# Kernel tuning notes

Hardware: AMD Instinct MI355X
Metric: run time of the kernel (lower is better)

The kernel has to match this reference:

```python
import jax, jax.numpy as jnp
import numpy as np

DIM = 1024
HEADS = 16
HEAD_DIM = DIM // HEADS
THRESH = 0.29514
SHARP = 15.0
LN_EPS = 1e-5
NORM_EPS = 1e-12


def setup_inputs() -> dict:
    key = jax.random.key(0)
    ks = jax.random.split(key, 8)
    s = 1.0 / np.sqrt(DIM)
    sg = 1.0 / np.sqrt(HEAD_DIM)
    return {
        "x": jax.random.normal(ks[0], (2, 2048, DIM), dtype=jnp.float32),
        "Wq": jax.random.uniform(ks[1], (DIM, DIM), jnp.float32, -s, s),
        "Wk": jax.random.uniform(ks[2], (DIM, DIM), jnp.float32, -s, s),
        "Wv": jax.random.uniform(ks[3], (DIM, DIM), jnp.float32, -s, s),
        "gq": jax.random.uniform(ks[4], (HEAD_DIM,), jnp.float32, -sg, sg),
        "gk": jax.random.uniform(ks[5], (HEAD_DIM,), jnp.float32, -sg, sg),
        "Wo": jax.random.uniform(ks[6], (DIM, DIM), jnp.float32, -s, s),
        "bo": jax.random.uniform(ks[7], (DIM,), jnp.float32, -s, s),
        "ln_w": jnp.ones((DIM,), jnp.float32),
        "ln_b": jnp.zeros((DIM,), jnp.float32),
    }


def _l2norm(t):
    # F.normalize: t / max(||t||_2, eps)
    n = jnp.sqrt(jnp.sum(t * t, axis=-1, keepdims=True))
    return t / jnp.maximum(n, NORM_EPS)


def reference(x, Wq, Wk, Wv, gq, gk, Wo, bo, ln_w, ln_b):
    B, T, D = x.shape
    # LayerNorm over last dim
    mu = jnp.mean(x, axis=-1, keepdims=True)
    var = jnp.mean((x - mu) ** 2, axis=-1, keepdims=True)
    x_norm = (x - mu) / jnp.sqrt(var + LN_EPS) * ln_w + ln_b

    def split_heads(t):  # [B,T,D] -> [B,H,T,hd]
        return t.reshape(B, T, HEADS, HEAD_DIM).transpose(0, 2, 1, 3)

    q = _l2norm(split_heads(x_norm @ Wq))
    k = _l2norm(split_heads(x_norm @ Wk))
    v = split_heads(x @ Wv)  # note: v uses un-normalized x, as in source

    align = jnp.einsum("bhtd,bhsd->bhts", q, k)  # cosine alignment
    resonance = jax.nn.sigmoid((align - THRESH) * SHARP)
    gate_q = jnp.einsum("bhtd,d->bht", q, gq)
    gate_k = jnp.einsum("bhsd,d->bhs", k, gk)
    modulation = resonance * gate_q[..., :, None] * gate_k[..., None, :]
    collapse = jnp.einsum("bhts,bhsd->bhtd", modulation, v)
    collapse = collapse.transpose(0, 2, 1, 3).reshape(B, T, D)
    return collapse @ Wo + bo
```

## Files before the change

### kernel.cpp

```cpp
#include <hip/hip_runtime.h>
#include <math.h>

#define DIM 1024
#define T_SEQ 2048
#define NBATCH 2
#define HEADS 16
#define HD 64
#define NTOK 4096
#define THRESH 0.29514f
#define SHARP 15.0f
#define LOG2E 1.4426950408889634f

typedef __attribute__((ext_vector_type(8))) short bf16x8;
typedef __attribute__((ext_vector_type(4))) float f32x4;
typedef __attribute__((ext_vector_type(4))) unsigned int u32x4;

__device__ __forceinline__ unsigned short f2b(float f) {
    unsigned int u = __float_as_uint(f);
    unsigned int r = (u + 0x7FFFu + ((u >> 16) & 1u)) >> 16;
    return (unsigned short)r;
}
__device__ __forceinline__ float b2f(unsigned short u) {
    return __uint_as_float(((unsigned int)u) << 16);
}
__device__ __forceinline__ unsigned int pack2_bf16(float lo, float hi) {
    unsigned int a = __float_as_uint(lo) + 0x8000u;
    unsigned int b = __float_as_uint(hi) + 0x8000u;
    return __builtin_amdgcn_perm(b, a, 0x07060302u);
}

__device__ __forceinline__ void async_cp16(const unsigned short* g, unsigned short* l) {
    __builtin_amdgcn_global_load_lds(
        (const __attribute__((address_space(1))) unsigned int*)g,
        (__attribute__((address_space(3))) unsigned int*)l, 16, 0, 0);
}

__global__ __launch_bounds__(256) void prep_kernel(
    const float* __restrict__ x, const float* __restrict__ lnw, const float* __restrict__ lnb,
    unsigned short* __restrict__ xnb, unsigned short* __restrict__ xb,
    const float* __restrict__ W0, const float* __restrict__ W1,
    const float* __restrict__ W2, const float* __restrict__ W3,
    unsigned short* __restrict__ T0, unsigned short* __restrict__ T1,
    unsigned short* __restrict__ T2, unsigned short* __restrict__ T3) {
    __shared__ float tile[64][65];
    if (blockIdx.x < 1024) {
        int row = blockIdx.x * 4 + (threadIdx.x >> 6);
        int lane = threadIdx.x & 63;
        const float4* xr = (const float4*)(x + (size_t)row * DIM);
        float4 v[4];
        float s = 0.f, ss = 0.f;
#pragma unroll
        for (int i = 0; i < 4; i++) {
            v[i] = xr[lane + i * 64];
            s += v[i].x + v[i].y + v[i].z + v[i].w;
            ss += v[i].x * v[i].x + v[i].y * v[i].y + v[i].z * v[i].z + v[i].w * v[i].w;
        }
#pragma unroll
        for (int off = 32; off; off >>= 1) {
            s += __shfl_xor(s, off);
            ss += __shfl_xor(ss, off);
        }
        float m = s * (1.f / DIM);
        float rstd = rsqrtf(ss * (1.f / DIM) - m * m + 1e-5f);
#pragma unroll
        for (int i = 0; i < 4; i++) {
            int e = (lane + i * 64) * 4;
            float4 lw = *(const float4*)&lnw[e];
            float4 lb = *(const float4*)&lnb[e];
            ushort4 un, ur;
            un.x = f2b((v[i].x - m) * rstd * lw.x + lb.x);
            un.y = f2b((v[i].y - m) * rstd * lw.y + lb.y);
            un.z = f2b((v[i].z - m) * rstd * lw.z + lb.z);
            un.w = f2b((v[i].w - m) * rstd * lw.w + lb.w);
            ur.x = f2b(v[i].x); ur.y = f2b(v[i].y); ur.z = f2b(v[i].z); ur.w = f2b(v[i].w);
            *(ushort4*)&xnb[(size_t)row * DIM + e] = un;
            *(ushort4*)&xb[(size_t)row * DIM + e] = ur;
        }
    } else {
        const int i = blockIdx.x - 1024;
        const int z = i >> 8;
        const int k0 = ((i >> 4) & 15) * 64, n0 = (i & 15) * 64;
        const float* W = (z == 0) ? W0 : (z == 1) ? W1 : (z == 2) ? W2 : W3;
        unsigned short* T = (z == 0) ? T0 : (z == 1) ? T1 : (z == 2) ? T2 : T3;
        const int r = threadIdx.x >> 3;
        const int c = (threadIdx.x & 7) * 8;
#pragma unroll
        for (int half = 0; half < 2; half++) {
            int rr = r + half * 32;
            float4 a = *(const float4*)&W[(size_t)(k0 + rr) * DIM + n0 + c];
            float4 b = *(const float4*)&W[(size_t)(k0 + rr) * DIM + n0 + c + 4];
            tile[rr][c + 0] = a.x; tile[rr][c + 1] = a.y; tile[rr][c + 2] = a.z; tile[rr][c + 3] = a.w;
            tile[rr][c + 4] = b.x; tile[rr][c + 5] = b.y; tile[rr][c + 6] = b.z; tile[rr][c + 7] = b.w;
        }
        __syncthreads();
#pragma unroll
        for (int half = 0; half < 2; half++) {
            int dd = r + half * 32;
            bf16x8 o;
#pragma unroll
            for (int j = 0; j < 8; j++) o[j] = (short)f2b(tile[c + j][dd]);
            *(bf16x8*)&T[(size_t)(n0 + dd) * DIM + k0 + c] = o;
        }
    }
}

template <int MODE>
__global__ __launch_bounds__(256) void gemm_mfma_kernel(
    const unsigned short* __restrict__ A0, const unsigned short* __restrict__ A2,
    const unsigned short* __restrict__ Bt0, const unsigned short* __restrict__ Bt1,
    const unsigned short* __restrict__ Bt2, const float* __restrict__ bias,
    const float* __restrict__ gq, const float* __restrict__ gk,
    unsigned short* __restrict__ Oq, unsigned short* __restrict__ Ok,
    unsigned short* __restrict__ Ov, float* __restrict__ gq_t, float* __restrict__ gk_t,
    float* __restrict__ Oout) {
    constexpr int NT = (MODE == 0) ? 4 : 2;
    constexpr int NBUF = (MODE == 0) ? 3 : 2;
    __shared__ __align__(16) unsigned short As[NBUF][128 * 32];
    __shared__ __align__(16) unsigned short Bs[NBUF][NT * 32 * 32];
    const int tid = threadIdx.x;
    const int lane = tid & 63, w = tid >> 6;
    const int l16 = lane & 15, quad = lane >> 4;
    const int wm = w >> 1, wn = w & 1;
    int m0, n0, z = 0;
    if constexpr (MODE == 0) {
        const int f = blockIdx.x + (blockIdx.y << 5) + (blockIdx.z << 8);
        const int ww = (f & 7) * 96 + (f >> 3);
        z = ww >> 8;
        m0 = ((ww >> 3) & 31) * 128;
        n0 = (ww & 7) * 128;
    } else {
        const int f = blockIdx.x + (blockIdx.y << 5);
        const int ww = (f & 7) * 64 + (f >> 3);
        m0 = (ww >> 4) * 128;
        n0 = (ww & 15) * 64;
    }
    const unsigned short* A;
    const unsigned short* Bt;
    if constexpr (MODE == 0) {
        A = (z == 2) ? A2 : A0;
        Bt = (z == 0) ? Bt0 : (z == 1) ? Bt1 : Bt2;
    } else {
        A = A0;
        Bt = Bt0;
    }
    f32x4 acc[4][NT] = {};
    const int kswz = (l16 >> 1) & 3;

    const int lin0 = tid, lin1 = 256 + tid;
    const int sm0 = lin0 >> 2, sk0 = (lin0 & 3) ^ ((sm0 >> 1) & 3);
    const int sm1 = lin1 >> 2, sk1 = (lin1 & 3) ^ ((sm1 >> 1) & 3);

    auto stage_async = [&](int kb, int k0) {
        async_cp16(Bt + (size_t)(n0 + sm0) * DIM + k0 + sk0 * 8, &Bs[kb][lin0 * 8]);
        if constexpr (MODE == 0) {
            async_cp16(Bt + (size_t)(n0 + sm1) * DIM + k0 + sk1 * 8, &Bs[kb][lin1 * 8]);
            async_cp16(A + (size_t)(m0 + sm0) * DIM + k0 + sk0 * 8, &As[kb][lin0 * 8]);
            async_cp16(A + (size_t)(m0 + sm1) * DIM + k0 + sk1 * 8, &As[kb][lin1 * 8]);
        }
    };

    bf16x8 pa0, pa1, pc0, pc1;
    auto loadA = [&](int k0) {
        const size_t o0 = (size_t)(m0 + sm0) * DIM + k0 + sk0 * 8;
        const size_t o1 = (size_t)(m0 + sm1) * DIM + k0 + sk1 * 8;
        pa0 = *(const bf16x8*)(A + o0);
        pc0 = *(const bf16x8*)(A2 + o0);
        pa1 = *(const bf16x8*)(A + o1);
        pc1 = *(const bf16x8*)(A2 + o1);
    };
    auto writeA = [&](int kb) {
        bf16x8 o0, o1;
#pragma unroll
        for (int j = 0; j < 8; j++) {
            o0[j] = (short)f2b(b2f((unsigned short)pa0[j]) + b2f((unsigned short)pc0[j]));
            o1[j] = (short)f2b(b2f((unsigned short)pa1[j]) + b2f((unsigned short)pc1[j]));
        }
        *(bf16x8*)(&As[kb][lin0 * 8]) = o0;
        *(bf16x8*)(&As[kb][lin1 * 8]) = o1;
    };

    auto compute = [&](int cur) {
        bf16x8 af[4], bfr[NT];
#pragma unroll
        for (int t = 0; t < 4; t++) {
            int ma = wm * 64 + t * 16 + l16;
            af[t] = *(const bf16x8*)(&As[cur][ma * 32 + ((quad ^ kswz) * 8)]);
        }
#pragma unroll
        for (int t = 0; t < NT; t++) {
            int nb = wn * (NT * 16) + t * 16 + l16;
            bfr[t] = *(const bf16x8*)(&Bs[cur][nb * 32 + ((quad ^ kswz) * 8)]);
        }
#pragma unroll
        for (int mt = 0; mt < 4; mt++)
#pragma unroll
            for (int nt = 0; nt < NT; nt++)
                acc[mt][nt] =
                    __builtin_amdgcn_mfma_f32_16x16x32_bf16(af[mt], bfr[nt], acc[mt][nt], 0, 0, 0);
    };

    if constexpr (MODE == 0) {
        stage_async(0, 0);
        stage_async(1, 32);
        int cur = 0, stg = 2;
        for (int ks = 0; ks < DIM / 32; ks++) {
            __builtin_amdgcn_s_barrier();
            if (ks + 2 < DIM / 32) {
                stage_async(stg, (ks + 2) * 32);
                asm volatile("s_waitcnt vmcnt(8)" ::: "memory");
            } else if (ks + 1 < DIM / 32) {
                asm volatile("s_waitcnt vmcnt(4)" ::: "memory");
            } else {
                asm volatile("s_waitcnt vmcnt(0)" ::: "memory");
            }
            __builtin_amdgcn_s_barrier();
            compute(cur);
            cur = (cur == 2) ? 0 : cur + 1;
            stg = (stg == 2) ? 0 : stg + 1;
        }
    } else {
        stage_async(0, 0);
        loadA(0);
        writeA(0);
        __syncthreads();
        for (int ks = 0; ks < DIM / 32; ks++) {
            const int cur = ks & 1;
            if (ks + 1 < DIM / 32) {
                stage_async(cur ^ 1, (ks + 1) * 32);
                loadA((ks + 1) * 32);
            }
            compute(cur);
            if (ks + 1 < DIM / 32) writeA(cur ^ 1);
            __syncthreads();
        }
    }

    if constexpr (MODE == 0) {
        const int h = (n0 + wn * 64) >> 6;
        if (z <= 1) {
            constexpr float QSCALE = -SHARP * LOG2E;
            const float* gvec = (z == 0) ? gq : gk;
            float* gate = (z == 0) ? gq_t : gk_t;
            unsigned short* O = (z == 0) ? Oq : Ok;
            const float oscale = (z == 0) ? QSCALE : 1.0f;
            float gv[4];
#pragma unroll
            for (int nt = 0; nt < 4; nt++) gv[nt] = gvec[nt * 16 + l16];
#pragma unroll
            for (int mt = 0; mt < 4; mt++) {
#pragma unroll
                for (int r = 0; r < 4; r++) {
                    float ss = 0.f;
#pragma unroll
                    for (int nt = 0; nt < 4; nt++) ss += acc[mt][nt][r] * acc[mt][nt][r];
#pragma unroll
                    for (int msk = 1; msk < 16; msk <<= 1) ss += __shfl_xor(ss, msk);
                    float rn = __builtin_amdgcn_rcpf(fmaxf(sqrtf(ss), 1e-12f));
                    float vn[4], gg = 0.f;
#pragma unroll
                    for (int nt = 0; nt < 4; nt++) {
                        vn[nt] = acc[mt][nt][r] * rn;
                        gg += vn[nt] * gv[nt];
                    }
#pragma unroll
                    for (int msk = 1; msk < 16; msk <<= 1) gg += __shfl_xor(gg, msk);
                    int tok = m0 + wm * 64 + mt * 16 + quad * 4 + r;
                    int b = tok >> 11, t = tok & 2047;
                    size_t rowbase = ((size_t)(b * HEADS + h) * T_SEQ + t) * HD;
#pragma unroll
                    for (int nt = 0; nt < 4; nt++)
                        O[rowbase + nt * 16 + l16] = f2b(vn[nt] * oscale);
                    if (l16 == 0) gate[(b * HEADS + h) * T_SEQ + t] = gg;
                }
            }
        } else {
#pragma unroll
            for (int mt = 0; mt < 4; mt++) {
#pragma unroll
                for (int r = 0; r < 4; r++) {
                    int tok = m0 + wm * 64 + mt * 16 + quad * 4 + r;
                    int b = tok >> 11, t = tok & 2047;
                    size_t rowbase = ((size_t)(b * HEADS + h) * T_SEQ + t) * HD;
#pragma unroll
                    for (int nt = 0; nt < 4; nt++)
                        Ov[rowbase + nt * 16 + l16] = f2b(acc[mt][nt][r]);
                }
            }
        }
    } else {
        float bias_r[NT];
#pragma unroll
        for (int nt = 0; nt < NT; nt++) bias_r[nt] = bias[n0 + wn * (NT * 16) + nt * 16 + l16];
#pragma unroll
        for (int mt = 0; mt < 4; mt++) {
#pragma unroll
            for (int r = 0; r < 4; r++) {
                int tok = m0 + wm * 64 + mt * 16 + quad * 4 + r;
#pragma unroll
                for (int nt = 0; nt < NT; nt++) {
                    int n = n0 + wn * (NT * 16) + nt * 16 + l16;
                    Oout[(size_t)tok * DIM + n] = acc[mt][nt][r] + bias_r[nt];
                }
            }
        }
    }
}

__global__ __launch_bounds__(256) void vtrans_kernel(const unsigned short* __restrict__ Vn,
                                                     const float* __restrict__ gk_t,
                                                     unsigned short* __restrict__ Vt) {
    __shared__ float tile[64][65];
    const int bh = blockIdx.y;
    const int t0 = blockIdx.x * 64;
    const int r = threadIdx.x >> 3;
    const int c = (threadIdx.x & 7) * 8;
    const unsigned short* src = Vn + (size_t)bh * T_SEQ * HD;
#pragma unroll
    for (int half = 0; half < 2; half++) {
        int rr = r + half * 32;
        float gkv = gk_t[bh * T_SEQ + t0 + rr];
        bf16x8 v = *(const bf16x8*)(src + (size_t)(t0 + rr) * HD + c);
#pragma unroll
        for (int j = 0; j < 8; j++) tile[rr][c + j] = b2f((unsigned short)v[j]) * gkv;
    }
    __syncthreads();
    unsigned short* dst = Vt + (size_t)bh * HD * T_SEQ;
#pragma unroll
    for (int half = 0; half < 2; half++) {
        int dd = r + half * 32;
        bf16x8 o;
#pragma unroll
        for (int j = 0; j < 8; j++) o[j] = (short)f2b(tile[c + j][dd]);
        *(bf16x8*)(dst + (size_t)dd * T_SEQ + t0 + c) = o;
    }
}

__global__ __launch_bounds__(256, 4) void attn_mfma_kernel(
    const unsigned short* __restrict__ Qn, const unsigned short* __restrict__ Kn,
    const unsigned short* __restrict__ Vt, const float* __restrict__ gateq,
    unsigned short* __restrict__ collp0, unsigned short* __restrict__ collp1) {
    __shared__ __align__(16) unsigned short Ks[2][64 * 64];
    __shared__ __align__(16) unsigned short VtL[2][64 * 64];
    const int tid = threadIdx.x;
    const int lane = tid & 63, w = tid >> 6;
    const int quad = lane >> 4, l16 = lane & 15;
    const int f = blockIdx.x + 16 * blockIdx.y + 256 * blockIdx.z;
    const int q_ = f >> 3;
    const int panel = (f & 7) * 8 + (q_ >> 4);
    const int t0 = (q_ & 15) * 128;
    const int h = panel & 15;
    const int zz = panel >> 4;
    const int b = zz >> 1, shalf = zz & 1;
    const int sbase = shalf * (T_SEQ / 2);
    const int bh = b * HEADS + h;
    const size_t base = (size_t)bh * T_SEQ * HD;
    constexpr float K0 = THRESH * SHARP * LOG2E;
    const f32x4 k0v = {K0, K0, K0, K0};

    int det0 = quad, det1 = quad + 4;
    asm("v_permlane16_swap_b32 %0, %1" : "+v"(det0), "+v"(det1));
    const bool flagA = (__builtin_amdgcn_readfirstlane(det0) == 0);

    bf16x8 fq[2][2];
#pragma unroll
    for (int mt = 0; mt < 2; mt++) {
        const unsigned short* qrow = Qn + base + (size_t)(t0 + w * 32 + mt * 16 + l16) * HD;
        fq[mt][0] = *(const bf16x8*)(qrow + quad * 8);
        fq[mt][1] = *(const bf16x8*)(qrow + 32 + quad * 8);
    }

    f32x4 oacc[4][2] = {};
    const int srow = tid >> 3;
    const int sgp = tid & 7;
    const int swz = l16 & 7;

    auto stage_chunk = [&](unsigned short* ksn, unsigned short* vtn, int s0) {
#pragma unroll
        for (int half = 0; half < 2; half++) {
            int row = srow + half * 32;
            int g = sgp ^ (row & 7);
            async_cp16(Kn + base + (size_t)(s0 + row) * HD + g * 8, ksn + row * 64 + sgp * 8);
            async_cp16(Vt + base + (size_t)row * T_SEQ + s0 + g * 8, vtn + row * 64 + sgp * 8);
        }
    };

    auto do_chunk = [&](const unsigned short* ksb, const unsigned short* vtb) {
#pragma unroll
        for (int kh = 0; kh < 2; kh++) {
            unsigned int p[2][2][2];
#pragma unroll
            for (int ct2 = 0; ct2 < 2; ct2++) {
                const int ct = 2 * kh + ct2;
                const unsigned short* krow = ksb + (ct * 16 + l16) * 64;
                bf16x8 fk0 = *(const bf16x8*)(krow + (quad ^ swz) * 8);
                bf16x8 fk1 = *(const bf16x8*)(krow + ((quad + 4) ^ swz) * 8);
#pragma unroll
                for (int mt = 0; mt < 2; mt++) {
                    __builtin_amdgcn_s_setprio(1);
                    f32x4 s1 =
                        __builtin_amdgcn_mfma_f32_16x16x32_bf16(fk0, fq[mt][0], k0v, 0, 0, 0);
                    f32x4 sacc =
                        __builtin_amdgcn_mfma_f32_16x16x32_bf16(fk1, fq[mt][1], s1, 0, 0, 0);
                    __builtin_amdgcn_s_setprio(0);
                    float w0 = __builtin_amdgcn_rcpf(1.f + __builtin_amdgcn_exp2f(sacc[0]));
                    float w1 = __builtin_amdgcn_rcpf(1.f + __builtin_amdgcn_exp2f(sacc[1]));
                    float w2 = __builtin_amdgcn_rcpf(1.f + __builtin_amdgcn_exp2f(sacc[2]));
                    float w3 = __builtin_amdgcn_rcpf(1.f + __builtin_amdgcn_exp2f(sacc[3]));
                    p[mt][ct2][0] = pack2_bf16(w0, w1);
                    p[mt][ct2][1] = pack2_bf16(w2, w3);
                }
            }
            int gv = (4 * kh + 2 * (quad & 1) + (quad >> 1)) ^ swz;
            bf16x8 fv[4];
#pragma unroll
            for (int dt = 0; dt < 4; dt++)
                fv[dt] = *(const bf16x8*)(vtb + (dt * 16 + l16) * 64 + gv * 8);
#pragma unroll
            for (int mt = 0; mt < 2; mt++) {
                unsigned int aL = p[mt][0][0], aH = p[mt][0][1];
                unsigned int bL = p[mt][1][0], bH = p[mt][1][1];
                asm("v_permlane16_swap_b32 %0, %1" : "+v"(aL), "+v"(bL));
                asm("v_permlane16_swap_b32 %0, %1" : "+v"(aH), "+v"(bH));
                u32x4 bt;
                if (flagA) {
                    bt.x = aL; bt.y = aH; bt.z = bL; bt.w = bH;
                } else {
                    bt.x = bL; bt.y = bH; bt.z = aL; bt.w = aH;
                }
                bf16x8 fs = __builtin_bit_cast(bf16x8, bt);
                __builtin_amdgcn_s_setprio(1);
#pragma unroll
                for (int dt = 0; dt < 4; dt++)
                    oacc[dt][mt] =
                        __builtin_amdgcn_mfma_f32_16x16x32_bf16(fv[dt], fs, oacc[dt][mt], 0, 0, 0);
                __builtin_amdgcn_s_setprio(0);
            }
        }
        __syncthreads();
    };

    stage_chunk(&Ks[0][0], &VtL[0][0], sbase);
    __syncthreads();

    for (int j = 0; j < T_SEQ / 256; j++) {
        stage_chunk(&Ks[1][0], &VtL[1][0], sbase + j * 128 + 64);
        do_chunk(&Ks[0][0], &VtL[0][0]);
        if (j + 1 < T_SEQ / 256) stage_chunk(&Ks[0][0], &VtL[0][0], sbase + j * 128 + 128);
        do_chunk(&Ks[1][0], &VtL[1][0]);
    }

    unsigned short* collp = shalf ? collp1 : collp0;
#pragma unroll
    for (int mt = 0; mt < 2; mt++) {
        int t = t0 + w * 32 + mt * 16 + l16;
        float gq_v = gateq[bh * T_SEQ + t];
        unsigned short* dst = collp + ((size_t)b * T_SEQ + t) * DIM + h * HD;
#pragma unroll
        for (int dt = 0; dt < 4; dt++) {
            ushort4 o;
            o.x = f2b(oacc[dt][mt][0] * gq_v);
            o.y = f2b(oacc[dt][mt][1] * gq_v);
            o.z = f2b(oacc[dt][mt][2] * gq_v);
            o.w = f2b(oacc[dt][mt][3] * gq_v);
            *(ushort4*)(dst + dt * 16 + quad * 4) = o;
        }
    }
}

extern "C" void kernel_launch(void* const* d_in, const int* in_sizes, int n_in,
                              void* d_out, int out_size, void* d_ws, size_t ws_size,
                              hipStream_t stream) {
    const float* x = (const float*)d_in[0];
    const float* Wq = (const float*)d_in[1];
    const float* Wk = (const float*)d_in[2];
    const float* Wv = (const float*)d_in[3];
    const float* gq = (const float*)d_in[4];
    const float* gk = (const float*)d_in[5];
    const float* Wo = (const float*)d_in[6];
    const float* bo = (const float*)d_in[7];
    const float* lnw = (const float*)d_in[8];
    const float* lnb = (const float*)d_in[9];
    float* out = (float*)d_out;

    unsigned short* ws = (unsigned short*)d_ws;
    unsigned short* xnb = ws;
    unsigned short* xb = xnb + (size_t)NTOK * DIM;
    unsigned short* Wqt = xb + (size_t)NTOK * DIM;
    unsigned short* Wkt = Wqt + (size_t)DIM * DIM;
    unsigned short* Wvt = Wkt + (size_t)DIM * DIM;
    unsigned short* Wot = Wvt + (size_t)DIM * DIM;
    unsigned short* Q16 = Wot + (size_t)DIM * DIM;
    unsigned short* K16 = Q16 + (size_t)NTOK * DIM;
    unsigned short* Vn = K16 + (size_t)NTOK * DIM;
    float* gq_t = (float*)(Vn + (size_t)NTOK * DIM);
    float* gk_t = gq_t + NBATCH * HEADS * T_SEQ;
    unsigned short* collb1 = (unsigned short*)(gk_t + NBATCH * HEADS * T_SEQ);
    unsigned short* Vt = xnb;
    unsigned short* collb0 = xb;

    prep_kernel<<<2048, 256, 0, stream>>>(x, lnw, lnb, xnb, xb, Wq, Wk, Wv, Wo, Wqt, Wkt, Wvt,
                                          Wot);
    gemm_mfma_kernel<0><<<dim3(NTOK / 128, DIM / 128, 3), 256, 0, stream>>>(
        xnb, xb, Wqt, Wkt, Wvt, nullptr, gq, gk, Q16, K16, Vn, gq_t, gk_t, nullptr);
    vtrans_kernel<<<dim3(T_SEQ / 64, NBATCH * HEADS), 256, 0, stream>>>(Vn, gk_t, Vt);
    attn_mfma_kernel<<<dim3(T_SEQ / 128, HEADS, NBATCH * 2), 256, 0, stream>>>(
        Q16, K16, Vt, gq_t, collb0, collb1);
    gemm_mfma_kernel<1><<<dim3(NTOK / 128, DIM / 64, 1), 256, 0, stream>>>(
        collb0, collb1, Wot, nullptr, nullptr, bo, nullptr, nullptr, nullptr, nullptr, nullptr,
        nullptr, nullptr, out);
}
```

Measured before the change: 222.1 us.

## Remove split-KV attention and partial-sum reduction in output projection GEMM

Attention blocks now iterate over the full key sequence instead of half, halving the grid and writing a single collapse buffer. The output-projection GEMM loads A via async copies directly rather than loading two partial buffers and adding them in registers. This removes the extra partial-buffer write/read and the add-on-load, at the cost of fewer attention blocks and lower parallelism/occupancy.

```diff
diff --git a/kernel.cpp b/kernel.cpp
--- a/kernel.cpp
+++ b/kernel.cpp
@@ -106,13 +106,13 @@
 
 template <int MODE>
 __global__ __launch_bounds__(256) void gemm_mfma_kernel(
-    const unsigned short* __restrict__ A0, const unsigned short* __restrict__ A2,
+    const unsigned short* __restrict__ A0,
     const unsigned short* __restrict__ Bt0, const unsigned short* __restrict__ Bt1,
     const unsigned short* __restrict__ Bt2, const float* __restrict__ bias,
     const float* __restrict__ gq, const float* __restrict__ gk,
     unsigned short* __restrict__ Oq, unsigned short* __restrict__ Ok,
     unsigned short* __restrict__ Ov, float* __restrict__ gq_t, float* __restrict__ gk_t,
-    float* __restrict__ Oout) {
+    float* __restrict__ Oout, const unsigned short* __restrict__ A2) {
     constexpr int NT = (MODE == 0) ? 4 : 2;
     constexpr int NBUF = (MODE == 0) ? 3 : 2;
     __shared__ __align__(16) unsigned short As[NBUF][128 * 32];
@@ -152,31 +152,10 @@
 
     auto stage_async = [&](int kb, int k0) {
         async_cp16(Bt + (size_t)(n0 + sm0) * DIM + k0 + sk0 * 8, &Bs[kb][lin0 * 8]);
-        if constexpr (MODE == 0) {
+        if constexpr (MODE == 0)
             async_cp16(Bt + (size_t)(n0 + sm1) * DIM + k0 + sk1 * 8, &Bs[kb][lin1 * 8]);
-            async_cp16(A + (size_t)(m0 + sm0) * DIM + k0 + sk0 * 8, &As[kb][lin0 * 8]);
-            async_cp16(A + (size_t)(m0 + sm1) * DIM + k0 + sk1 * 8, &As[kb][lin1 * 8]);
-        }
-    };
-
-    bf16x8 pa0, pa1, pc0, pc1;
-    auto loadA = [&](int k0) {
-        const size_t o0 = (size_t)(m0 + sm0) * DIM + k0 + sk0 * 8;
-        const size_t o1 = (size_t)(m0 + sm1) * DIM + k0 + sk1 * 8;
-        pa0 = *(const bf16x8*)(A + o0);
-        pc0 = *(const bf16x8*)(A2 + o0);
-        pa1 = *(const bf16x8*)(A + o1);
-        pc1 = *(const bf16x8*)(A2 + o1);
-    };
-    auto writeA = [&](int kb) {
-        bf16x8 o0, o1;
-#pragma unroll
-        for (int j = 0; j < 8; j++) {
-            o0[j] = (short)f2b(b2f((unsigned short)pa0[j]) + b2f((unsigned short)pc0[j]));
-            o1[j] = (short)f2b(b2f((unsigned short)pa1[j]) + b2f((unsigned short)pc1[j]));
-        }
-        *(bf16x8*)(&As[kb][lin0 * 8]) = o0;
-        *(bf16x8*)(&As[kb][lin1 * 8]) = o1;
+        async_cp16(A + (size_t)(m0 + sm0) * DIM + k0 + sk0 * 8, &As[kb][lin0 * 8]);
+        async_cp16(A + (size_t)(m0 + sm1) * DIM + k0 + sk1 * 8, &As[kb][lin1 * 8]);
     };
 
     auto compute = [&](int cur) {
@@ -220,17 +199,11 @@
         }
     } else {
         stage_async(0, 0);
-        loadA(0);
-        writeA(0);
         __syncthreads();
         for (int ks = 0; ks < DIM / 32; ks++) {
             const int cur = ks & 1;
-            if (ks + 1 < DIM / 32) {
-                stage_async(cur ^ 1, (ks + 1) * 32);
-                loadA((ks + 1) * 32);
-            }
+            if (ks + 1 < DIM / 32) stage_async(cur ^ 1, (ks + 1) * 32);
             compute(cur);
-            if (ks + 1 < DIM / 32) writeA(cur ^ 1);
             __syncthreads();
         }
     }
@@ -338,7 +311,7 @@
 __global__ __launch_bounds__(256, 4) void attn_mfma_kernel(
     const unsigned short* __restrict__ Qn, const unsigned short* __restrict__ Kn,
     const unsigned short* __restrict__ Vt, const float* __restrict__ gateq,
-    unsigned short* __restrict__ collp0, unsigned short* __restrict__ collp1) {
+    unsigned short* __restrict__ coll) {
     __shared__ __align__(16) unsigned short Ks[2][64 * 64];
     __shared__ __align__(16) unsigned short VtL[2][64 * 64];
     const int tid = threadIdx.x;
@@ -346,12 +319,10 @@
     const int quad = lane >> 4, l16 = lane & 15;
     const int f = blockIdx.x + 16 * blockIdx.y + 256 * blockIdx.z;
     const int q_ = f >> 3;
-    const int panel = (f & 7) * 8 + (q_ >> 4);
+    const int panel = (f & 7) * 4 + (q_ >> 4);
     const int t0 = (q_ & 15) * 128;
     const int h = panel & 15;
-    const int zz = panel >> 4;
-    const int b = zz >> 1, shalf = zz & 1;
-    const int sbase = shalf * (T_SEQ / 2);
+    const int b = panel >> 4;
     const int bh = b * HEADS + h;
     const size_t base = (size_t)bh * T_SEQ * HD;
     constexpr float K0 = THRESH * SHARP * LOG2E;
@@ -439,22 +410,21 @@
         __syncthreads();
     };
 
-    stage_chunk(&Ks[0][0], &VtL[0][0], sbase);
+    stage_chunk(&Ks[0][0], &VtL[0][0], 0);
     __syncthreads();
 
-    for (int j = 0; j < T_SEQ / 256; j++) {
-        stage_chunk(&Ks[1][0], &VtL[1][0], sbase + j * 128 + 64);
+    for (int j = 0; j < T_SEQ / 128; j++) {
+        stage_chunk(&Ks[1][0], &VtL[1][0], j * 128 + 64);
         do_chunk(&Ks[0][0], &VtL[0][0]);
-        if (j + 1 < T_SEQ / 256) stage_chunk(&Ks[0][0], &VtL[0][0], sbase + j * 128 + 128);
+        if (j + 1 < T_SEQ / 128) stage_chunk(&Ks[0][0], &VtL[0][0], j * 128 + 128);
         do_chunk(&Ks[1][0], &VtL[1][0]);
     }
 
-    unsigned short* collp = shalf ? collp1 : collp0;
 #pragma unroll
     for (int mt = 0; mt < 2; mt++) {
         int t = t0 + w * 32 + mt * 16 + l16;
         float gq_v = gateq[bh * T_SEQ + t];
-        unsigned short* dst = collp + ((size_t)b * T_SEQ + t) * DIM + h * HD;
+        unsigned short* dst = coll + ((size_t)b * T_SEQ + t) * DIM + h * HD;
 #pragma unroll
         for (int dt = 0; dt < 4; dt++) {
             ushort4 o;
@@ -494,18 +464,16 @@
     unsigned short* Vn = K16 + (size_t)NTOK * DIM;
     float* gq_t = (float*)(Vn + (size_t)NTOK * DIM);
     float* gk_t = gq_t + NBATCH * HEADS * T_SEQ;
-    unsigned short* collb1 = (unsigned short*)(gk_t + NBATCH * HEADS * T_SEQ);
     unsigned short* Vt = xnb;
-    unsigned short* collb0 = xb;
+    unsigned short* coll = xb;
 
     prep_kernel<<<2048, 256, 0, stream>>>(x, lnw, lnb, xnb, xb, Wq, Wk, Wv, Wo, Wqt, Wkt, Wvt,
                                           Wot);
     gemm_mfma_kernel<0><<<dim3(NTOK / 128, DIM / 128, 3), 256, 0, stream>>>(
-        xnb, xb, Wqt, Wkt, Wvt, nullptr, gq, gk, Q16, K16, Vn, gq_t, gk_t, nullptr);
+        xnb, Wqt, Wkt, Wvt, nullptr, gq, gk, Q16, K16, Vn, gq_t, gk_t, nullptr, xb);
     vtrans_kernel<<<dim3(T_SEQ / 64, NBATCH * HEADS), 256, 0, stream>>>(Vn, gk_t, Vt);
-    attn_mfma_kernel<<<dim3(T_SEQ / 128, HEADS, NBATCH * 2), 256, 0, stream>>>(
-        Q16, K16, Vt, gq_t, collb0, collb1);
+    attn_mfma_kernel<<<dim3(16, 16, 2), 256, 0, stream>>>(Q16, K16, Vt, gq_t, coll);
     gemm_mfma_kernel<1><<<dim3(NTOK / 128, DIM / 64, 1), 256, 0, stream>>>(
-        collb0, collb1, Wot, nullptr, nullptr, bo, nullptr, nullptr, nullptr, nullptr, nullptr,
-        nullptr, nullptr, out);
-}
+        coll, Wot, nullptr, nullptr, bo, nullptr, nullptr, nullptr, nullptr, nullptr, nullptr,
+        nullptr, out, nullptr);
+}
```

New measurement: 213.4 us (median of 2 runs). 1.04x faster.
